# Optimization experiments

Measured on AMD Instinct MI355X. Metric: run time of the kernel, lower is better.

The kernel has to match this reference:

```python
import jax, jax.numpy as jnp
import numpy as np


def setup_inputs() -> dict:
    key = jax.random.key(0)
    ks = jax.random.split(key, 8)
    B, L, DIM, INNER = 4, 4096, 1024, 512
    return {
        "x": jax.random.normal(ks[0], (B, L, DIM), dtype=jnp.float32),
        "w_a": jax.random.normal(ks[1], (2 * INNER, DIM), dtype=jnp.float32) * (DIM ** -0.5),
        "w_x": jax.random.normal(ks[2], (2 * INNER, DIM), dtype=jnp.float32) * (DIM ** -0.5),
        "w_out": jax.random.normal(ks[3], (DIM, INNER), dtype=jnp.float32) * (INNER ** -0.5),
        "mat_v_real": jax.random.normal(ks[4], (INNER, INNER), dtype=jnp.float32),
        "mat_v_imag": jax.random.normal(ks[5], (INNER, INNER), dtype=jnp.float32),
        "last_hidden_real": jax.random.normal(ks[6], (INNER,), dtype=jnp.float32),
        "last_hidden_imag": jax.random.normal(ks[7], (INNER,), dtype=jnp.float32),
    }


def reference(x, w_a, w_x, w_out, mat_v_real, mat_v_imag,
              last_hidden_real, last_hidden_imag):
    b, l, dim = x.shape
    inner = mat_v_real.shape[0]
    V = jax.lax.complex(mat_v_real, mat_v_imag)          # (inner, inner)
    Vinv = jnp.linalg.inv(V)
    h0 = jax.lax.complex(last_hidden_real, last_hidden_imag)  # (inner,)

    xf = x.astype(jnp.float32)
    # decay gate a: complex, |a| = sigmoid(log|a_raw|^2) < 1
    a2 = (xf @ w_a.T).reshape(b, l, inner, 2)
    a_mag2 = a2[..., 0] ** 2 + a2[..., 1] ** 2
    a = jax.lax.complex(a2[..., 0], a2[..., 1]) * (
        jax.lax.rsqrt(a_mag2) * jax.nn.sigmoid(jnp.log(a_mag2)))

    # input projection: x_c <- x_c * |x_c|  (rsqrt(m)*m == sqrt(m))
    x2 = (xf @ w_x.T).reshape(b, l, inner, 2)
    x_mag2 = x2[..., 0] ** 2 + x2[..., 1] ** 2
    xc = jax.lax.complex(x2[..., 0], x2[..., 1]) * (jax.lax.rsqrt(x_mag2) * x_mag2)

    # x_roll[t] = xc[t-1], x_roll[0] = last_hidden (broadcast over batch)
    x_roll = jnp.concatenate(
        [jnp.broadcast_to(h0, (b, 1, inner)), xc[:, :-1]], axis=1)

    # Original builds c[l,m] = prod_{k=l..m} a_k via FFT cumsum of logs, then
    # V diag(c) V^{-1} contracted with x_roll. Equivalent diagonal recurrence:
    #   u_t = V^{-1} x_roll_t ;  s_t = a_t * s_{t-1} + a_t * u_t ;  h_t = V s_t + xc_t
    u = jnp.einsum('mn,bln->blm', Vinv, x_roll)

    def combine(c1, c2):
        a1, b1 = c1
        a2_, b2 = c2
        return (a2_ * a1, a2_ * b1 + b2)

    _, s = jax.lax.associative_scan(combine, (a, a * u), axis=1)
    h = jnp.einsum('mn,bln->blm', V, s) + xc                 # (b, l, inner) complex
    return (h.real @ w_out.T).astype(x.dtype)                # (b, l, dim)
```

## Files before the change

### kernel.cpp

```cpp
#include <hip/hip_runtime.h>

typedef unsigned short u16;
typedef short bf16x8 __attribute__((ext_vector_type(8)));
typedef float f32x4 __attribute__((ext_vector_type(4)));

typedef const __attribute__((address_space(1))) void* gaddr_t;
typedef __attribute__((address_space(3))) void* laddr_t;

__device__ __forceinline__ u16 f2b(float f){
  unsigned u = __float_as_uint(f);
  u = (u + 0x7fffu + ((u >> 16) & 1u)) >> 16;
  return (u16)u;
}
__device__ __forceinline__ float b2f(u16 h){
  return __uint_as_float(((unsigned)h) << 16);
}

__global__ void cast_all(const float* __restrict__ x, const float* __restrict__ wa,
                         const float* __restrict__ wx, const float* __restrict__ wo,
                         u16* __restrict__ Xb, u16* __restrict__ WAb,
                         u16* __restrict__ WXb, u16* __restrict__ WOb){
  int i = blockIdx.x*blockDim.x + threadIdx.x;
  int st = gridDim.x*blockDim.x;
  for (int idx = i; idx < 4849664; idx += st){
    const float* s; u16* d; int o;
    if (idx < 4194304){ s = x; d = Xb; o = idx; }
    else if (idx < 4456448){ s = wa; d = WAb; o = idx - 4194304; }
    else if (idx < 4718592){ s = wx; d = WXb; o = idx - 4456448; }
    else { s = wo; d = WOb; o = idx - 4718592; }
    float4 v = ((const float4*)s)[o];
    ushort4 r; r.x=f2b(v.x); r.y=f2b(v.y); r.z=f2b(v.z); r.w=f2b(v.w);
    ((ushort4*)d)[o] = r;
  }
}

__global__ void inv_init(const float* __restrict__ vr, const float* __restrict__ vi,
                         float2* __restrict__ aug, float2* __restrict__ prow){
  int idx = blockIdx.x*256 + threadIdx.x;
  int r = idx >> 10, c = idx & 1023;
  float2 v;
  if (c < 512) v = make_float2(vr[r*512+c], vi[r*512+c]);
  else         v = make_float2((c-512)==r ? 1.f : 0.f, 0.f);
  aug[idx] = v;
  if (r < 32 && c >= 32) prow[idx] = v;
}

__global__ __launch_bounds__(64) void inv_panel(const float2* __restrict__ aug, int bs,
                                                float2* __restrict__ binv){
  const int lane = threadIdx.x;
  float tx[32], ty[32];
  #pragma unroll
  for (int r = 0; r < 32; ++r){
    if (lane < 32){
      float2 v = aug[(size_t)(bs+r)*1024 + bs + lane];
      tx[r] = v.x; ty[r] = v.y;
    } else {
      tx[r] = ((lane-32)==r) ? 1.f : 0.f; ty[r] = 0.f;
    }
  }
  #pragma unroll
  for (int k = 0; k < 32; ++k){
    float px = __shfl(tx[k], k), py = __shfl(ty[k], k);
    float dkk = px*px + py*py;
    if (dkk < 1e-8f){
      float bm = -1.f; int bp = k;
      #pragma unroll
      for (int r = k; r < 32; ++r){
        float m2 = tx[r]*tx[r] + ty[r]*ty[r];
        if (m2 > bm){ bm = m2; bp = r; }
      }
      int p = __shfl(bp, k);
      if (p != k){
        float okx = tx[k], oky = ty[k];
        float spx = okx, spy = oky;
        #pragma unroll
        for (int r = 1; r < 32; ++r){ if (r > k && r == p){ spx = tx[r]; spy = ty[r]; } }
        #pragma unroll
        for (int r = 1; r < 32; ++r){ if (r > k && r == p){ tx[r] = okx; ty[r] = oky; } }
        tx[k] = spx; ty[k] = spy;
        px = __shfl(spx, k); py = __shfl(spy, k);
        dkk = px*px + py*py;
      }
    }
    float dinv = 1.f / dkk;
    float pvx = px*dinv, pvy = -py*dinv;
    float nx = tx[k]*pvx - ty[k]*pvy;
    float ny = tx[k]*pvy + ty[k]*pvx;
    tx[k] = nx; ty[k] = ny;
    #pragma unroll
    for (int r = 0; r < 32; ++r){
      if (r == k) continue;
      float fx = __shfl(tx[r], k), fy = __shfl(ty[r], k);
      tx[r] -= fx*nx - fy*ny;
      ty[r] -= fx*ny + fy*nx;
    }
  }
  if (lane >= 32){
    #pragma unroll
    for (int r = 0; r < 32; ++r)
      binv[r*32 + (lane-32)] = make_float2(tx[r], ty[r]);
  }
}

__global__ __launch_bounds__(256) void inv_update(float2* __restrict__ aug, int bs,
    const float2* __restrict__ prow, float2* __restrict__ prow_next,
    const float2* __restrict__ binv){
  __shared__ float2 Bi[32][33];
  __shared__ float2 Pr[32][33];
  __shared__ float2 T1[32][33];
  __shared__ float2 Pc[128][33];
  const int tid = threadIdx.x;
  const int c0 = bs + 32 + blockIdx.x*32;
  const int r0 = blockIdx.y*128;
  for (int idx = tid; idx < 1024; idx += 256){
    Bi[idx>>5][idx&31] = binv[idx];
    Pr[idx>>5][idx&31] = prow[(size_t)(idx>>5)*1024 + c0 + (idx&31)];
  }
  for (int idx = tid; idx < 128*32; idx += 256){
    int rr = idx>>5, j = idx&31;
    Pc[rr][j] = aug[(size_t)(r0+rr)*1024 + bs + j];
  }
  __syncthreads();
  for (int idx = tid; idx < 1024; idx += 256){
    int j = idx>>5, cc2 = idx&31;
    float2 acc = make_float2(0.f, 0.f);
    #pragma unroll
    for (int kk = 0; kk < 32; ++kk){
      float2 bv = Bi[j][kk], sv = Pr[kk][cc2];
      acc.x += bv.x*sv.x - bv.y*sv.y;
      acc.y += bv.x*sv.y + bv.y*sv.x;
    }
    T1[j][cc2] = acc;
  }
  __syncthreads();
  const int cc = tid & 31;
  float2 t1c[32];
  #pragma unroll
  for (int j = 0; j < 32; ++j) t1c[j] = T1[j][cc];
  #pragma unroll 4
  for (int i = 0; i < 16; ++i){
    int idx = tid + i*256;
    int rr = idx>>5;
    int r = r0+rr, c = c0+cc;
    float2 nv;
    if (r >= bs && r < bs+32){
      nv = T1[r-bs][cc];
    } else {
      nv = aug[(size_t)r*1024 + c];
      #pragma unroll
      for (int j = 0; j < 32; ++j){
        float2 pq = Pc[rr][j], t = t1c[j];
        nv.x -= pq.x*t.x - pq.y*t.y;
        nv.y -= pq.x*t.y + pq.y*t.x;
      }
    }
    aug[(size_t)r*1024 + c] = nv;
    int rn = r - (bs+32);
    if (rn >= 0 && rn < 32) prow_next[(size_t)rn*1024 + c] = nv;
  }
}

__global__ void build_minv(const float2* __restrict__ aug, u16* __restrict__ Mi){
  int idx = blockIdx.x*256 + threadIdx.x;
  int row = idx >> 10, col = idx & 1023;
  int m = row >> 1, irow = row & 1;
  int k = col & 511, icol = col >> 9;
  float2 a = aug[(size_t)m*1024 + 512 + k];
  float v;
  if (!irow) v = icol ? -a.y : a.x;
  else       v = icol ?  a.x : a.y;
  Mi[idx] = f2b(v);
}
__global__ void build_mv4(const float* __restrict__ vr, const float* __restrict__ vi,
                          u16* __restrict__ Mv){
  int idx = blockIdx.x*256 + threadIdx.x;
  int m = idx >> 10, col = idx & 1023;
  int n = col >> 1;
  float v = (col & 1) ? -vi[m*512+n] : vr[m*512+n];
  Mv[idx] = f2b(v);
}
__global__ void fill_h0(const float* __restrict__ lhr, const float* __restrict__ lhi,
                        u16* __restrict__ xroll){
  int idx = blockIdx.x*256 + threadIdx.x;
  int b = idx >> 10, c = idx & 1023;
  float v = (c < 512) ? lhr[c] : lhi[c-512];
  xroll[(size_t)b*4096*1024 + c] = f2b(v);
}

enum { EPI_BF16 = 0, EPI_A = 1, EPI_X = 2, EPI_ADDXC = 3, EPI_OUTF32 = 4 };

#define MFMA_BF16(a,b,c) __builtin_amdgcn_mfma_f32_16x16x32_bf16(a,b,c,0,0,0)

template<int EPI>
__global__ __launch_bounds__(512, 2) void gemm256(
    const u16* __restrict__ A, const u16* __restrict__ B,
    int K, int NT, int N,
    void* __restrict__ C, void* __restrict__ aux0, void* __restrict__ aux1)
{
  extern __shared__ u16 LDS[];
  const int tid = threadIdx.x;
  const int w = tid >> 6, lane = tid & 63;
  const int wm = w >> 2, wn = w & 3;
  const int fr = lane & 15, kg = lane >> 4;

  const int cpx = gridDim.x >> 3;
  const int bid = blockIdx.x;
  const int swz = (bid & 7)*cpx + (bid >> 3);
  const int bx = swz & 63, by = swz >> 6;
  const size_t arow0 = (size_t)bx * 256;
  const int bcol0 = by * 256;

  const int rL = w*16 + (lane >> 2);
  const int glog = (lane & 3) ^ ((lane >> 3) & 3);
  const u16* Asrc = A + (arow0 + rL)*(size_t)K + glog*8;
  const u16* Bsrc = B + ((size_t)(bcol0 + rL))*K + glog*8;
  const size_t KH = (size_t)128 * K;
  const int sdst = w*512;

  const int goff = (kg ^ ((fr >> 1) & 3)) * 8;
  const int aro = wm*4096 + fr*32 + goff;
  const int bro = 32768 + (wn>>1)*4096 + (wn&1)*2048 + fr*32 + goff;

  f32x4 acc[8][4] = {};
  bf16x8 bfr[4];

  auto STG_A = [&](int kt){
    int bo = (kt & 3)*8192;
    #pragma unroll
    for (int h = 0; h < 2; ++h)
      __builtin_amdgcn_global_load_lds((gaddr_t)(Asrc + h*KH + kt*32),
          (laddr_t)(LDS + bo + h*4096 + sdst), 16, 0, 0);
  };
  auto STG_B = [&](int kt){
    int bo = 32768 + (kt & 3)*8192;
    #pragma unroll
    for (int h = 0; h < 2; ++h)
      __builtin_amdgcn_global_load_lds((gaddr_t)(Bsrc + h*KH + kt*32),
          (laddr_t)(LDS + bo + h*4096 + sdst), 16, 0, 0);
  };

  auto TILE = [&](int kt, int stg, int wait){
    const int ab = (kt & 3)*8192 + aro;
    const int bb = (kt & 3)*8192 + bro;
    bf16x8 af[4];
    #pragma unroll
    for (int m = 0; m < 4; ++m) af[m] = *(const bf16x8*)&LDS[ab + m*512];
    #pragma unroll
    for (int n = 0; n < 4; ++n) bfr[n] = *(const bf16x8*)&LDS[bb + n*512];
    if (stg) STG_A(kt + 3);
    __builtin_amdgcn_s_barrier();
    __builtin_amdgcn_s_setprio(1);
    #pragma unroll
    for (int m = 0; m < 4; ++m)
      #pragma unroll
      for (int n = 0; n < 4; ++n)
        acc[m][n] = MFMA_BF16(af[m], bfr[n], acc[m][n]);
    __builtin_amdgcn_s_setprio(0);
    __builtin_amdgcn_s_barrier();
    #pragma unroll
    for (int m = 0; m < 4; ++m) af[m] = *(const bf16x8*)&LDS[ab + (m+4)*512];
    if (stg) STG_B(kt + 3);
    __builtin_amdgcn_s_barrier();
    __builtin_amdgcn_s_setprio(1);
    #pragma unroll
    for (int m = 0; m < 4; ++m)
      #pragma unroll
      for (int n = 0; n < 4; ++n)
        acc[m+4][n] = MFMA_BF16(af[m], bfr[n], acc[m+4][n]);
    __builtin_amdgcn_s_setprio(0);
    if (wait == 2){ asm volatile("s_waitcnt vmcnt(8)" ::: "memory"); }
    else if (wait == 1){ asm volatile("s_waitcnt vmcnt(4)" ::: "memory"); }
    else if (wait == 0){ asm volatile("s_waitcnt vmcnt(0)" ::: "memory"); }
    __builtin_amdgcn_sched_barrier(0);
    __builtin_amdgcn_s_barrier();
  };

  STG_A(0); STG_B(0); STG_A(1); STG_B(1); STG_A(2); STG_B(2);
  asm volatile("s_waitcnt vmcnt(8)" ::: "memory");
  __builtin_amdgcn_sched_barrier(0);
  __builtin_amdgcn_s_barrier();

  #pragma unroll 1
  for (int kt = 0; kt < NT - 3; ++kt) TILE(kt, 1, 2);
  TILE(NT-3, 0, 1);
  TILE(NT-2, 0, 0);
  TILE(NT-1, 0, -1);

  const int rbase = wm*128 + (lane >> 4)*4;
  const int cbase = wn*64 + fr;
  #pragma unroll
  for (int M = 0; M < 8; ++M){
    #pragma unroll
    for (int Np = 0; Np < 4; ++Np){
      #pragma unroll
      for (int j = 0; j < 4; ++j){
        float v = acc[M][Np][j];
        size_t gr = arow0 + rbase + M*16 + j;
        int gc = bcol0 + cbase + Np*16;
        if constexpr (EPI == EPI_BF16){
          ((u16*)C)[gr*(size_t)N + gc] = f2b(v);
        } else if constexpr (EPI == EPI_OUTF32){
          ((float*)C)[gr*(size_t)N + gc] = v;
        } else if constexpr (EPI == EPI_ADDXC){
          float xc = b2f(((const u16*)aux0)[gr*512 + gc]);
          ((u16*)C)[gr*512 + gc] = f2b(v + xc);
        } else {
          float pv = __shfl_xor(v, 1);
          int odd = lane & 1;
          float re = odd ? pv : v;
          float im = odd ? v : pv;
          float m2 = re*re + im*im;
          int mh = gc >> 1;
          if constexpr (EPI == EPI_A){
            float sc = m2 > 0.f ? sqrtf(m2)/(1.f + m2) : 0.f;
            if (!odd){
              unsigned pk = (unsigned)f2b(re*sc) | ((unsigned)f2b(im*sc) << 16);
              ((unsigned*)aux0)[gr*512 + mh] = pk;
            }
          } else {
            float sc = sqrtf(m2);
            u16 ob = f2b(v * sc);
            if (!odd) ((u16*)aux0)[gr*512 + mh] = ob;
            int t = (int)(gr & 4095);
            if (t != 4095)
              ((u16*)aux1)[(gr+1)*1024 + (odd ? 512 + mh : mh)] = ob;
          }
        }
      }
    }
  }
}

__global__ void scan_p1(const unsigned* __restrict__ aint, const unsigned* __restrict__ uint_,
                        float4* __restrict__ agg){
  int idx = blockIdx.x*256 + threadIdx.x;
  int m = idx & 511, chunk = (idx >> 9) & 63, b = idx >> 15;
  size_t row = (size_t)b*4096 + chunk*64;
  float px=1.f, py=0.f, sx=0.f, sy=0.f;
  for (int i = 0; i < 64; ++i, ++row){
    unsigned av = aint[row*512 + m];
    unsigned uv = uint_[row*512 + m];
    float ar = b2f((u16)av), ai = b2f((u16)(av>>16));
    float ur = b2f((u16)uv), ui = b2f((u16)(uv>>16));
    float tx2 = sx + ur, ty2 = sy + ui;
    sx = ar*tx2 - ai*ty2; sy = ar*ty2 + ai*tx2;
    float np = px*ar - py*ai; py = px*ai + py*ar; px = np;
  }
  agg[((size_t)(b*512+m))*64 + chunk] = make_float4(px,py,sx,sy);
}
__global__ void scan_p2(const float4* __restrict__ agg, float2* __restrict__ carry){
  int seq = blockIdx.x*256 + threadIdx.x;
  float sx = 0.f, sy = 0.f;
  for (int c = 0; c < 64; ++c){
    carry[(size_t)seq*64 + c] = make_float2(sx, sy);
    float4 g = agg[(size_t)seq*64 + c];
    float nx = g.x*sx - g.y*sy + g.z;
    sy = g.x*sy + g.y*sx + g.w; sx = nx;
  }
}
__global__ void scan_p3(const unsigned* __restrict__ aint, const unsigned* __restrict__ uint_,
                        const float2* __restrict__ carry, unsigned* __restrict__ sout){
  int idx = blockIdx.x*256 + threadIdx.x;
  int m = idx & 511, chunk = (idx >> 9) & 63, b = idx >> 15;
  size_t row = (size_t)b*4096 + chunk*64;
  float2 c0 = carry[((size_t)(b*512+m))*64 + chunk];
  float sx = c0.x, sy = c0.y;
  for (int i = 0; i < 64; ++i, ++row){
    unsigned av = aint[row*512 + m];
    unsigned uv = uint_[row*512 + m];
    float ar = b2f((u16)av), ai = b2f((u16)(av>>16));
    float ur = b2f((u16)uv), ui = b2f((u16)(uv>>16));
    float tx2 = sx + ur, ty2 = sy + ui;
    sx = ar*tx2 - ai*ty2; sy = ar*ty2 + ai*tx2;
    sout[row*512 + m] = (unsigned)f2b(sx) | ((unsigned)f2b(sy) << 16);
  }
}

extern "C" void kernel_launch(void* const* d_in, const int* in_sizes, int n_in,
                              void* d_out, int out_size, void* d_ws, size_t ws_size,
                              hipStream_t stream){
  (void)in_sizes; (void)n_in; (void)out_size; (void)ws_size;
  const float* x   = (const float*)d_in[0];
  const float* wa  = (const float*)d_in[1];
  const float* wx  = (const float*)d_in[2];
  const float* wo  = (const float*)d_in[3];
  const float* vr  = (const float*)d_in[4];
  const float* vi  = (const float*)d_in[5];
  const float* lhr = (const float*)d_in[6];
  const float* lhi = (const float*)d_in[7];

  char* ws = (char*)d_ws;
  const size_t SB = 16384ull*1024*2;
  const size_t HB = SB/2;
  u16* Xb    = (u16*)(ws);
  unsigned* AINT = (unsigned*)(ws + SB);
  u16* XROLL = (u16*)(ws + 2*SB);
  u16* XCRE  = (u16*)(ws + 3*SB);
  char* p = ws + 3*SB + HB;
  u16* WAb   = (u16*)p; p += 2097152;
  u16* WXb   = (u16*)p; p += 2097152;
  u16* MINV  = (u16*)p; p += 2097152;
  u16* MV4   = (u16*)p; p += 1048576;
  u16* WOUTb = (u16*)p; p += 1048576;
  float2* AUG   = (float2*)p; p += 4194304;
  float2* PROWA = (float2*)p; p += 262144;
  float2* PROWB = (float2*)p; p += 262144;
  float2* BINV  = (float2*)p; p += 8192;
  float4* AGG   = (float4*)p; p += 2048ull*64*16;
  float2* CARRY = (float2*)p; p += 2048ull*64*8;
  u16* U   = Xb;
  u16* S   = XROLL;
  u16* HRE = (u16*)AINT;

  cast_all<<<2048,256,0,stream>>>(x, wa, wx, wo, Xb, WAb, WXb, WOUTb);

  inv_init<<<2048,256,0,stream>>>(vr, vi, AUG, PROWA);
  float2* pr = PROWA; float2* prn = PROWB;
  for (int bs = 0; bs < 512; bs += 32){
    inv_panel<<<1,64,0,stream>>>(AUG, bs, BINV);
    inv_update<<<dim3((992-bs)/32, 4),256,0,stream>>>(AUG, bs, pr, prn, BINV);
    float2* t = pr; pr = prn; prn = t;
  }
  build_minv<<<4096,256,0,stream>>>(AUG, MINV);
  build_mv4<<<2048,256,0,stream>>>(vr, vi, MV4);

  const size_t GLDS = 131072;
  gemm256<EPI_A><<<256,512,GLDS,stream>>>(Xb, WAb, 1024, 32, 1024, nullptr, (void*)AINT, nullptr);
  gemm256<EPI_X><<<256,512,GLDS,stream>>>(Xb, WXb, 1024, 32, 1024, nullptr, (void*)XCRE, (void*)XROLL);
  fill_h0<<<16,256,0,stream>>>(lhr, lhi, XROLL);
  gemm256<EPI_BF16><<<256,512,GLDS,stream>>>(XROLL, MINV, 1024, 32, 1024, (void*)U, nullptr, nullptr);

  scan_p1<<<512,256,0,stream>>>((const unsigned*)AINT, (const unsigned*)U, AGG);
  scan_p2<<<8,256,0,stream>>>(AGG, CARRY);
  scan_p3<<<512,256,0,stream>>>((const unsigned*)AINT, (const unsigned*)U, CARRY, (unsigned*)S);

  gemm256<EPI_ADDXC><<<128,512,GLDS,stream>>>(S, MV4, 1024, 32, 512, (void*)HRE, (void*)XCRE, nullptr);
  gemm256<EPI_OUTF32><<<256,512,GLDS,stream>>>(HRE, WOUTb, 512, 16, 1024, d_out, nullptr, nullptr);
}
```

Measured before the change: 1.390 ms.

## Fuse gate and input projection GEMMs and fold panel inversion into update kernel

Concatenates w_a and w_x into one weight buffer so a single GEMM with N=2048 produces both the decay gate and the input projection, and the epilogue picks its output by column range. The per-step 32x32 panel Gauss-Jordan inverse moves from a separate one-wave kernel into the inv_update kernel. One designated block computes the next panel's inverse in LDS with 256 threads, using parallel pivot search and double-buffered binv. This removes 16 tiny serial kernel launches and one GEMM launch and reads X once for both projections. In exchange, that one block in each update does extra serial work, and the grid swizzle is now parameterized by byShift.

```diff
diff --git a/kernel.cpp b/kernel.cpp
--- a/kernel.cpp
+++ b/kernel.cpp
@@ -15,18 +15,21 @@
 __device__ __forceinline__ float b2f(u16 h){
   return __uint_as_float(((unsigned)h) << 16);
 }
+__device__ __forceinline__ float2 cmul(float2 a, float2 b){
+  return make_float2(a.x*b.x - a.y*b.y, a.x*b.y + a.y*b.x);
+}
 
 __global__ void cast_all(const float* __restrict__ x, const float* __restrict__ wa,
                          const float* __restrict__ wx, const float* __restrict__ wo,
-                         u16* __restrict__ Xb, u16* __restrict__ WAb,
-                         u16* __restrict__ WXb, u16* __restrict__ WOb){
+                         u16* __restrict__ Xb, u16* __restrict__ WABb,
+                         u16* __restrict__ WOb){
   int i = blockIdx.x*blockDim.x + threadIdx.x;
   int st = gridDim.x*blockDim.x;
   for (int idx = i; idx < 4849664; idx += st){
     const float* s; u16* d; int o;
     if (idx < 4194304){ s = x; d = Xb; o = idx; }
-    else if (idx < 4456448){ s = wa; d = WAb; o = idx - 4194304; }
-    else if (idx < 4718592){ s = wx; d = WXb; o = idx - 4456448; }
+    else if (idx < 4456448){ s = wa; d = WABb; o = idx - 4194304; }
+    else if (idx < 4718592){ s = wx; d = WABb + 1048576; o = idx - 4456448; }
     else { s = wo; d = WOb; o = idx - 4718592; }
     float4 v = ((const float4*)s)[o];
     ushort4 r; r.x=f2b(v.x); r.y=f2b(v.y); r.z=f2b(v.z); r.w=f2b(v.w);
@@ -45,75 +48,88 @@
   if (r < 32 && c >= 32) prow[idx] = v;
 }
 
-__global__ __launch_bounds__(64) void inv_panel(const float2* __restrict__ aug, int bs,
-                                                float2* __restrict__ binv){
-  const int lane = threadIdx.x;
-  float tx[32], ty[32];
-  #pragma unroll
-  for (int r = 0; r < 32; ++r){
-    if (lane < 32){
-      float2 v = aug[(size_t)(bs+r)*1024 + bs + lane];
-      tx[r] = v.x; ty[r] = v.y;
-    } else {
-      tx[r] = ((lane-32)==r) ? 1.f : 0.f; ty[r] = 0.f;
-    }
-  }
-  #pragma unroll
+__device__ __forceinline__ void gj32(float2 (&L)[32][33], float2 (&R)[32][33],
+                                     float2* fcol, int tid){
   for (int k = 0; k < 32; ++k){
-    float px = __shfl(tx[k], k), py = __shfl(ty[k], k);
-    float dkk = px*px + py*py;
-    if (dkk < 1e-8f){
-      float bm = -1.f; int bp = k;
+    if (tid < 64){
+      int lane = tid;
+      float2 colv = make_float2(0.f, 0.f);
+      float mag = -1.f;
+      if (lane < 32){
+        colv = L[lane][k];
+        if (lane >= k) mag = colv.x*colv.x + colv.y*colv.y;
+      }
+      int best = lane;
       #pragma unroll
-      for (int r = k; r < 32; ++r){
-        float m2 = tx[r]*tx[r] + ty[r]*ty[r];
-        if (m2 > bm){ bm = m2; bp = r; }
-      }
-      int p = __shfl(bp, k);
-      if (p != k){
-        float okx = tx[k], oky = ty[k];
-        float spx = okx, spy = oky;
-        #pragma unroll
-        for (int r = 1; r < 32; ++r){ if (r > k && r == p){ spx = tx[r]; spy = ty[r]; } }
-        #pragma unroll
-        for (int r = 1; r < 32; ++r){ if (r > k && r == p){ tx[r] = okx; ty[r] = oky; } }
-        tx[k] = spx; ty[k] = spy;
-        px = __shfl(spx, k); py = __shfl(spy, k);
-        dkk = px*px + py*py;
-      }
-    }
-    float dinv = 1.f / dkk;
-    float pvx = px*dinv, pvy = -py*dinv;
-    float nx = tx[k]*pvx - ty[k]*pvy;
-    float ny = tx[k]*pvy + ty[k]*pvx;
-    tx[k] = nx; ty[k] = ny;
-    #pragma unroll
-    for (int r = 0; r < 32; ++r){
-      if (r == k) continue;
-      float fx = __shfl(tx[r], k), fy = __shfl(ty[r], k);
-      tx[r] -= fx*nx - fy*ny;
-      ty[r] -= fx*ny + fy*nx;
-    }
-  }
-  if (lane >= 32){
-    #pragma unroll
-    for (int r = 0; r < 32; ++r)
-      binv[r*32 + (lane-32)] = make_float2(tx[r], ty[r]);
-  }
+      for (int off = 1; off < 32; off <<= 1){
+        float om = __shfl_xor(mag, off);
+        int ob  = __shfl_xor(best, off);
+        if (om > mag || (om == mag && ob < best)){ mag = om; best = ob; }
+      }
+      int p = __shfl(best, 0);
+      float pvx = __shfl(colv.x, p), pvy = __shfl(colv.y, p);
+      float dinv = 1.f / (pvx*pvx + pvy*pvy);
+      float2 pinv = make_float2(pvx*dinv, -pvy*dinv);
+      float2 rk = (lane < 32) ? L[k][lane] : R[k][lane-32];
+      float2 rp = (lane < 32) ? L[p][lane] : R[p][lane-32];
+      float2 nk = cmul(rp, pinv);
+      if (lane < 32) L[k][lane] = nk; else R[k][lane-32] = nk;
+      if (p != k){ if (lane < 32) L[p][lane] = rk; else R[p][lane-32] = rk; }
+      if (lane < 32){
+        float2 f = colv;
+        float okx = __shfl(colv.x, k), oky = __shfl(colv.y, k);
+        if (lane == p){ f.x = okx; f.y = oky; }
+        fcol[lane] = f;
+      }
+    }
+    __syncthreads();
+    #pragma unroll
+    for (int i = 0; i < 8; ++i){
+      int idx = tid + i*256;
+      int r = idx >> 6, c = idx & 63;
+      if (r != k){
+        float2 f = fcol[r];
+        float2 nk = (c < 32) ? L[k][c] : R[k][c-32];
+        float2 cell = (c < 32) ? L[r][c] : R[r][c-32];
+        cell.x -= f.x*nk.x - f.y*nk.y;
+        cell.y -= f.x*nk.y + f.y*nk.x;
+        if (c < 32) L[r][c] = cell; else R[r][c-32] = cell;
+      }
+    }
+    __syncthreads();
+  }
+}
+
+__global__ __launch_bounds__(256) void inv_panel0(const float2* __restrict__ aug,
+                                                  float2* __restrict__ binv){
+  __shared__ float2 L[32][33];
+  __shared__ float2 R[32][33];
+  __shared__ float2 fcol[32];
+  const int tid = threadIdx.x;
+  for (int i = tid; i < 1024; i += 256){
+    int r = i >> 5, c = i & 31;
+    L[r][c] = aug[(size_t)r*1024 + c];
+    R[r][c] = make_float2((r==c) ? 1.f : 0.f, 0.f);
+  }
+  __syncthreads();
+  gj32(L, R, fcol, tid);
+  for (int i = tid; i < 1024; i += 256) binv[i] = R[i>>5][i&31];
 }
 
 __global__ __launch_bounds__(256) void inv_update(float2* __restrict__ aug, int bs,
     const float2* __restrict__ prow, float2* __restrict__ prow_next,
-    const float2* __restrict__ binv){
+    const float2* __restrict__ binv_in, float2* __restrict__ binv_out, int do_panel){
   __shared__ float2 Bi[32][33];
   __shared__ float2 Pr[32][33];
   __shared__ float2 T1[32][33];
   __shared__ float2 Pc[128][33];
+  __shared__ float2 fcol[32];
   const int tid = threadIdx.x;
   const int c0 = bs + 32 + blockIdx.x*32;
   const int r0 = blockIdx.y*128;
+  const bool panel = do_panel && (blockIdx.x == 0) && ((int)blockIdx.y == ((bs+32) >> 7));
   for (int idx = tid; idx < 1024; idx += 256){
-    Bi[idx>>5][idx&31] = binv[idx];
+    Bi[idx>>5][idx&31] = binv_in[idx];
     Pr[idx>>5][idx&31] = prow[(size_t)(idx>>5)*1024 + c0 + (idx&31)];
   }
   for (int idx = tid; idx < 128*32; idx += 256){
@@ -137,6 +153,7 @@
   float2 t1c[32];
   #pragma unroll
   for (int j = 0; j < 32; ++j) t1c[j] = T1[j][cc];
+  __syncthreads();
   #pragma unroll 4
   for (int i = 0; i < 16; ++i){
     int idx = tid + i*256;
@@ -156,7 +173,20 @@
     }
     aug[(size_t)r*1024 + c] = nv;
     int rn = r - (bs+32);
-    if (rn >= 0 && rn < 32) prow_next[(size_t)rn*1024 + c] = nv;
+    if (rn >= 0 && rn < 32){
+      prow_next[(size_t)rn*1024 + c] = nv;
+      if (panel) Bi[rn][cc] = nv;
+    }
+  }
+  if (panel){
+    __syncthreads();
+    for (int i = tid; i < 1024; i += 256){
+      int r = i>>5, c = i&31;
+      Pr[r][c] = make_float2((r==c) ? 1.f : 0.f, 0.f);
+    }
+    __syncthreads();
+    gj32(Bi, Pr, fcol, tid);
+    for (int i = tid; i < 1024; i += 256) binv_out[i] = Pr[i>>5][i&31];
   }
 }
 
@@ -187,15 +217,16 @@
   xroll[(size_t)b*4096*1024 + c] = f2b(v);
 }
 
-enum { EPI_BF16 = 0, EPI_A = 1, EPI_X = 2, EPI_ADDXC = 3, EPI_OUTF32 = 4 };
+enum { EPI_BF16 = 0, EPI_ADDXC = 3, EPI_OUTF32 = 4, EPI_AX = 5 };
 
 #define MFMA_BF16(a,b,c) __builtin_amdgcn_mfma_f32_16x16x32_bf16(a,b,c,0,0,0)
 
 template<int EPI>
 __global__ __launch_bounds__(512, 2) void gemm256(
     const u16* __restrict__ A, const u16* __restrict__ B,
-    int K, int NT, int N,
-    void* __restrict__ C, void* __restrict__ aux0, void* __restrict__ aux1)
+    int K, int NT, int N, int byShift,
+    void* __restrict__ C, void* __restrict__ aux0, void* __restrict__ aux1,
+    void* __restrict__ aux2)
 {
   extern __shared__ u16 LDS[];
   const int tid = threadIdx.x;
@@ -206,7 +237,7 @@
   const int cpx = gridDim.x >> 3;
   const int bid = blockIdx.x;
   const int swz = (bid & 7)*cpx + (bid >> 3);
-  const int bx = swz & 63, by = swz >> 6;
+  const int by = swz & ((1 << byShift) - 1), bx = swz >> byShift;
   const size_t arow0 = (size_t)bx * 256;
   const int bcol0 = by * 256;
 
@@ -310,20 +341,21 @@
           float re = odd ? pv : v;
           float im = odd ? v : pv;
           float m2 = re*re + im*im;
-          int mh = gc >> 1;
-          if constexpr (EPI == EPI_A){
+          if (gc < 1024){
+            int mh = gc >> 1;
             float sc = m2 > 0.f ? sqrtf(m2)/(1.f + m2) : 0.f;
             if (!odd){
               unsigned pk = (unsigned)f2b(re*sc) | ((unsigned)f2b(im*sc) << 16);
               ((unsigned*)aux0)[gr*512 + mh] = pk;
             }
           } else {
+            int mh = (gc - 1024) >> 1;
             float sc = sqrtf(m2);
             u16 ob = f2b(v * sc);
-            if (!odd) ((u16*)aux0)[gr*512 + mh] = ob;
+            if (!odd) ((u16*)aux1)[gr*512 + mh] = ob;
             int t = (int)(gr & 4095);
             if (t != 4095)
-              ((u16*)aux1)[(gr+1)*1024 + (odd ? 512 + mh : mh)] = ob;
+              ((u16*)aux2)[(gr+1)*1024 + (odd ? 512 + mh : mh)] = ob;
           }
         }
       }
@@ -397,43 +429,50 @@
   u16* XROLL = (u16*)(ws + 2*SB);
   u16* XCRE  = (u16*)(ws + 3*SB);
   char* p = ws + 3*SB + HB;
-  u16* WAb   = (u16*)p; p += 2097152;
-  u16* WXb   = (u16*)p; p += 2097152;
+  u16* WABb  = (u16*)p; p += 4194304;
   u16* MINV  = (u16*)p; p += 2097152;
   u16* MV4   = (u16*)p; p += 1048576;
   u16* WOUTb = (u16*)p; p += 1048576;
   float2* AUG   = (float2*)p; p += 4194304;
   float2* PROWA = (float2*)p; p += 262144;
   float2* PROWB = (float2*)p; p += 262144;
-  float2* BINV  = (float2*)p; p += 8192;
+  float2* BINV0 = (float2*)p; p += 8192;
+  float2* BINV1 = (float2*)p; p += 8192;
   float4* AGG   = (float4*)p; p += 2048ull*64*16;
   float2* CARRY = (float2*)p; p += 2048ull*64*8;
   u16* U   = Xb;
   u16* S   = XROLL;
   u16* HRE = (u16*)AINT;
 
-  cast_all<<<2048,256,0,stream>>>(x, wa, wx, wo, Xb, WAb, WXb, WOUTb);
+  cast_all<<<2048,256,0,stream>>>(x, wa, wx, wo, Xb, WABb, WOUTb);
 
   inv_init<<<2048,256,0,stream>>>(vr, vi, AUG, PROWA);
+  inv_panel0<<<1,256,0,stream>>>(AUG, BINV0);
   float2* pr = PROWA; float2* prn = PROWB;
   for (int bs = 0; bs < 512; bs += 32){
-    inv_panel<<<1,64,0,stream>>>(AUG, bs, BINV);
-    inv_update<<<dim3((992-bs)/32, 4),256,0,stream>>>(AUG, bs, pr, prn, BINV);
+    int step = bs >> 5;
+    float2* bin  = (step & 1) ? BINV1 : BINV0;
+    float2* bout = (step & 1) ? BINV0 : BINV1;
+    inv_update<<<dim3((992-bs)/32, 4),256,0,stream>>>(AUG, bs, pr, prn, bin, bout,
+                                                      bs < 480 ? 1 : 0);
     float2* t = pr; pr = prn; prn = t;
   }
   build_minv<<<4096,256,0,stream>>>(AUG, MINV);
   build_mv4<<<2048,256,0,stream>>>(vr, vi, MV4);
+  fill_h0<<<16,256,0,stream>>>(lhr, lhi, XROLL);
 
   const size_t GLDS = 131072;
-  gemm256<EPI_A><<<256,512,GLDS,stream>>>(Xb, WAb, 1024, 32, 1024, nullptr, (void*)AINT, nullptr);
-  gemm256<EPI_X><<<256,512,GLDS,stream>>>(Xb, WXb, 1024, 32, 1024, nullptr, (void*)XCRE, (void*)XROLL);
-  fill_h0<<<16,256,0,stream>>>(lhr, lhi, XROLL);
-  gemm256<EPI_BF16><<<256,512,GLDS,stream>>>(XROLL, MINV, 1024, 32, 1024, (void*)U, nullptr, nullptr);
+  gemm256<EPI_AX><<<512,512,GLDS,stream>>>(Xb, WABb, 1024, 32, 2048, 3,
+                                           nullptr, (void*)AINT, (void*)XCRE, (void*)XROLL);
+  gemm256<EPI_BF16><<<256,512,GLDS,stream>>>(XROLL, MINV, 1024, 32, 1024, 2,
+                                             (void*)U, nullptr, nullptr, nullptr);
 
   scan_p1<<<512,256,0,stream>>>((const unsigned*)AINT, (const unsigned*)U, AGG);
   scan_p2<<<8,256,0,stream>>>(AGG, CARRY);
   scan_p3<<<512,256,0,stream>>>((const unsigned*)AINT, (const unsigned*)U, CARRY, (unsigned*)S);
 
-  gemm256<EPI_ADDXC><<<128,512,GLDS,stream>>>(S, MV4, 1024, 32, 512, (void*)HRE, (void*)XCRE, nullptr);
-  gemm256<EPI_OUTF32><<<256,512,GLDS,stream>>>(HRE, WOUTb, 512, 16, 1024, d_out, nullptr, nullptr);
-}
+  gemm256<EPI_ADDXC><<<128,512,GLDS,stream>>>(S, MV4, 1024, 32, 512, 1,
+                                              (void*)HRE, (void*)XCRE, nullptr, nullptr);
+  gemm256<EPI_OUTF32><<<256,512,GLDS,stream>>>(HRE, WOUTb, 512, 16, 1024, 2,
+                                               d_out, nullptr, nullptr, nullptr);
+}
```

After: 1.300 ms. 6.5% less time.
